# Kernel optimization log

Hardware: AMD Instinct MI355X
Metric: run time of the kernel (lower is better)

The kernel has to match this reference:

```python
import jax, jax.numpy as jnp
import numpy as np

N = 100000  # nodes
E = 1600000  # edges
F_IN, F_HID, F_OUT = 64, 128, 128


def _glorot(key, shape):
    fan_in, fan_out = shape[1], shape[0]
    lim = float(np.sqrt(6.0 / (fan_in + fan_out)))
    return jax.random.uniform(key, shape, jnp.float32, -lim, lim)


def setup_inputs() -> dict:
    key = jax.random.key(0)
    ks = jax.random.split(key, 8)
    x = jax.random.normal(ks[0], (N, F_IN), jnp.float32)
    edge_index = jax.random.randint(ks[1], (2, E), 0, N, jnp.int64)
    # SAGEConv params: lin_l (neighbors, with bias), lin_r (root, no bias)
    return {
        "x": x,
        "edge_index": edge_index,
        "W1_l": _glorot(ks[2], (F_HID, F_IN)),
        "b1": jnp.zeros((F_HID,), jnp.float32),
        "W1_r": _glorot(ks[3], (F_HID, F_IN)),
        "W2_l": _glorot(ks[4], (F_OUT, F_HID)),
        "b2": jnp.zeros((F_OUT,), jnp.float32),
        "W2_r": _glorot(ks[5], (F_OUT, F_HID)),
    }


def _sage_conv(x, src, dst, deg_inv, W_l, b, W_r):
    # mean aggregation of source features onto target nodes
    agg = jax.ops.segment_sum(x[src], dst, num_segments=N)  # [N, F]
    agg = agg * deg_inv[:, None]
    return agg @ W_l.T + b + x @ W_r.T


def reference(x, edge_index, W1_l, b1, W1_r, W2_l, b2, W2_r):
    src, dst = edge_index[0], edge_index[1]
    deg = jax.ops.segment_sum(jnp.ones((E,), jnp.float32), dst, num_segments=N)
    deg_inv = 1.0 / jnp.maximum(deg, 1.0)
    h = _sage_conv(x, src, dst, deg_inv, W1_l, b1, W1_r)
    h = jax.nn.relu(h)
    # dropout p=0.5 is identity in eval mode
    out = _sage_conv(h, src, dst, deg_inv, W2_l, b2, W2_r)
    return out
```

## Files before the change

kernel.cpp:

```cpp
#include <hip/hip_runtime.h>
#include <hip/hip_bf16.h>

__device__ __forceinline__ float b2f(unsigned short u) {
  return __uint_as_float(((unsigned int)u) << 16);
}
__device__ __forceinline__ unsigned short f2b(float f) {
  unsigned int x = __float_as_uint(f);
  unsigned int r = x + 0x7FFFu + ((x >> 16) & 1u);
  return (unsigned short)(r >> 16);
}
__device__ __forceinline__ unsigned int pack2(float lo, float hi) {
  return (unsigned int)f2b(lo) | ((unsigned int)f2b(hi) << 16);
}
__device__ __forceinline__ void acc8(float* a, uint4 p) {
  a[0] += __uint_as_float(p.x << 16); a[1] += __uint_as_float(p.x & 0xFFFF0000u);
  a[2] += __uint_as_float(p.y << 16); a[3] += __uint_as_float(p.y & 0xFFFF0000u);
  a[4] += __uint_as_float(p.z << 16); a[5] += __uint_as_float(p.z & 0xFFFF0000u);
  a[6] += __uint_as_float(p.w << 16); a[7] += __uint_as_float(p.w & 0xFFFF0000u);
}

typedef short bf16x8 __attribute__((ext_vector_type(8)));
typedef float f32x4 __attribute__((ext_vector_type(4)));

#define CHUNK 8192
#define NBUCKP 1024

__global__ void detect_kernel(const void* __restrict__ x_raw,
                              const void* __restrict__ idx_raw,
                              int* __restrict__ hdr) {
  int lane = threadIdx.x;
  const unsigned short* xb = (const unsigned short*)x_raw;
  unsigned short u = xb[2 * lane];
  int e = (u >> 7) & 0xFF;
  bool sane = ((u & 0x7FFFu) == 0) || (e >= 107 && e <= 137);
  unsigned long long m = __ballot(sane);
  const int* ib = (const int*)idx_raw;
  int v = ib[2 * lane + 1];
  unsigned long long m2 = __ballot(v != 0);
  if (lane == 0) {
    hdr[0] = (__popcll(m) >= 32) ? 0 : 1;
    hdr[1] = (m2 == 0ull) ? 1 : 0;
  }
}

__global__ void convert_w_kernel(const void* __restrict__ W1l, const void* __restrict__ W1r,
                                 const void* __restrict__ W2l, const void* __restrict__ W2r,
                                 const void* __restrict__ b1, const void* __restrict__ b2,
                                 const int* __restrict__ hdr,
                                 unsigned short* __restrict__ W1l_h, unsigned short* __restrict__ W1r_h,
                                 unsigned short* __restrict__ W2l_h, unsigned short* __restrict__ W2r_h,
                                 float* __restrict__ b1_f, float* __restrict__ b2_f) {
  int i = blockIdx.x * blockDim.x + threadIdx.x;
  const void* s; unsigned short* dh = nullptr; float* df = nullptr; int off;
  if (i < 8192)       { s = W1l; dh = W1l_h; off = i; }
  else if (i < 16384) { s = W1r; dh = W1r_h; off = i - 8192; }
  else if (i < 32768) { s = W2l; dh = W2l_h; off = i - 16384; }
  else if (i < 49152) { s = W2r; dh = W2r_h; off = i - 32768; }
  else if (i < 49280) { s = b1;  df = b1_f;  off = i - 49152; }
  else if (i < 49408) { s = b2;  df = b2_f;  off = i - 49280; }
  else return;
  float v = hdr[0] ? ((const float*)s)[off] : b2f(((const unsigned short*)s)[off]);
  if (dh) dh[off] = f2b(v);
  else df[off] = v;
}

__global__ void convert_x_kernel(const void* __restrict__ x_raw,
                                 const int* __restrict__ hdr,
                                 unsigned short* __restrict__ xc, int n_elems) {
  int i = blockIdx.x * blockDim.x + threadIdx.x;
  if (i >= n_elems) return;
  xc[i] = hdr[0] ? f2b(((const float*)x_raw)[i]) : ((const unsigned short*)x_raw)[i];
}

__global__ __launch_bounds__(256) void hist_chunks_kernel(
    const int* __restrict__ idx_raw, const int* __restrict__ hdr,
    int* __restrict__ H, int n_edges, int NC) {
  __shared__ int h[NBUCKP];
  for (int i = threadIdx.x; i < NBUCKP; i += 256) h[i] = 0;
  __syncthreads();
  const int c = blockIdx.x;
  const int base = c * CHUNK;
  const int lim = min(n_edges - base, CHUNK);
  if (hdr[1]) {
    const uint4* dp = (const uint4*)(idx_raw + 2 * (size_t)n_edges + 2 * (size_t)base);
    #pragma unroll
    for (int t = 0; t < CHUNK / 512; ++t) {
      int q = t * 256 + threadIdx.x;
      int e = 2 * q;
      if (e < lim) {
        uint4 v = dp[q];
        atomicAdd(&h[((int)v.x) >> 7], 1);
        if (e + 1 < lim) atomicAdd(&h[((int)v.z) >> 7], 1);
      }
    }
  } else {
    const uint4* dp = (const uint4*)(idx_raw + (size_t)n_edges + base);
    #pragma unroll
    for (int t = 0; t < CHUNK / 1024; ++t) {
      int q = t * 256 + threadIdx.x;
      int e = 4 * q;
      if (e < lim) {
        uint4 v = dp[q];
        atomicAdd(&h[((int)v.x) >> 7], 1);
        if (e + 1 < lim) atomicAdd(&h[((int)v.y) >> 7], 1);
        if (e + 2 < lim) atomicAdd(&h[((int)v.z) >> 7], 1);
        if (e + 3 < lim) atomicAdd(&h[((int)v.w) >> 7], 1);
      }
    }
  }
  __syncthreads();
  for (int i = threadIdx.x; i < NBUCKP; i += 256) H[(size_t)i * NC + c] = h[i];
}

__global__ __launch_bounds__(256) void gscan_sums_kernel(const int* __restrict__ arr,
                                                         int* __restrict__ blockSums, int n) {
  __shared__ int ws[4];
  int tid = threadIdx.x, lane = tid & 63, wid = tid >> 6;
  int base = blockIdx.x * 2048 + tid * 8;
  int s = 0;
  #pragma unroll
  for (int t = 0; t < 8; ++t) {
    int i = base + t;
    if (i < n) s += arr[i];
  }
  #pragma unroll
  for (int m = 1; m < 64; m <<= 1) s += __shfl_xor(s, m, 64);
  if (lane == 0) ws[wid] = s;
  __syncthreads();
  if (tid == 0) blockSums[blockIdx.x] = ws[0] + ws[1] + ws[2] + ws[3];
}

__global__ void gscan_offsets_kernel(const int* __restrict__ blockSums,
                                     int* __restrict__ blockOffs, int nb) {
  int lane = threadIdx.x;
  int carry = 0;
  for (int start = 0; start < nb; start += 64) {
    int i = start + lane;
    int v = (i < nb) ? blockSums[i] : 0;
    int isc = v;
    #pragma unroll
    for (int off = 1; off < 64; off <<= 1) {
      int t = __shfl_up(isc, off, 64);
      if (lane >= off) isc += t;
    }
    if (i < nb) blockOffs[i] = carry + isc - v;
    carry += __shfl(isc, 63, 64);
  }
}

__global__ __launch_bounds__(256) void gscan_emit_kernel(const int* __restrict__ arr,
                                                         const int* __restrict__ blockOffs,
                                                         int* __restrict__ out, int n) {
  __shared__ int ws[4];
  int tid = threadIdx.x, lane = tid & 63, wid = tid >> 6;
  int base = blockIdx.x * 2048 + tid * 8;
  int v[8];
  int s = 0;
  #pragma unroll
  for (int t = 0; t < 8; ++t) {
    int i = base + t;
    v[t] = (i < n) ? arr[i] : 0;
    s += v[t];
  }
  int isc = s;
  #pragma unroll
  for (int off = 1; off < 64; off <<= 1) {
    int t = __shfl_up(isc, off, 64);
    if (lane >= off) isc += t;
  }
  if (lane == 63) ws[wid] = isc;
  __syncthreads();
  int wb = 0;
  #pragma unroll
  for (int w = 0; w < 4; ++w)
    if (w < wid) wb += ws[w];
  int excl = blockOffs[blockIdx.x] + wb + isc - s;
  #pragma unroll
  for (int t = 0; t < 8; ++t) {
    int i = base + t;
    if (i < n) {
      out[i] = excl;
      excl += v[t];
    }
  }
}

__global__ __launch_bounds__(256) void scatter_kernel(
    const int* __restrict__ idx_raw, const int* __restrict__ hdr,
    const int* __restrict__ O, unsigned long long* __restrict__ ebuf,
    int n_edges, int NC) {
  __shared__ int base[NBUCKP];
  const int c = blockIdx.x;
  for (int i = threadIdx.x; i < NBUCKP; i += 256) base[i] = O[(size_t)i * NC + c];
  __syncthreads();
  const int eb = c * CHUNK;
  const int lim = min(n_edges - eb, CHUNK);
  if (hdr[1]) {
    const uint4* sp = (const uint4*)(idx_raw + 2 * (size_t)eb);
    const uint4* dp = (const uint4*)(idx_raw + 2 * (size_t)n_edges + 2 * (size_t)eb);
    #pragma unroll
    for (int t = 0; t < CHUNK / 512; ++t) {
      int q = t * 256 + threadIdx.x;
      int e = 2 * q;
      if (e < lim) {
        uint4 sv = sp[q], dv = dp[q];
        int p0 = atomicAdd(&base[((int)dv.x) >> 7], 1);
        ebuf[p0] = (unsigned long long)sv.x | ((unsigned long long)dv.x << 32);
        if (e + 1 < lim) {
          int p1 = atomicAdd(&base[((int)dv.z) >> 7], 1);
          ebuf[p1] = (unsigned long long)sv.z | ((unsigned long long)dv.z << 32);
        }
      }
    }
  } else {
    const uint4* sp = (const uint4*)(idx_raw + (size_t)eb);
    const uint4* dp = (const uint4*)(idx_raw + (size_t)n_edges + eb);
    #pragma unroll
    for (int t = 0; t < CHUNK / 1024; ++t) {
      int q = t * 256 + threadIdx.x;
      int e = 4 * q;
      if (e < lim) {
        uint4 sv = sp[q], dv = dp[q];
        int p0 = atomicAdd(&base[((int)dv.x) >> 7], 1);
        ebuf[p0] = (unsigned long long)sv.x | ((unsigned long long)dv.x << 32);
        if (e + 1 < lim) {
          int p1 = atomicAdd(&base[((int)dv.y) >> 7], 1);
          ebuf[p1] = (unsigned long long)sv.y | ((unsigned long long)dv.y << 32);
        }
        if (e + 2 < lim) {
          int p2 = atomicAdd(&base[((int)dv.z) >> 7], 1);
          ebuf[p2] = (unsigned long long)sv.z | ((unsigned long long)dv.z << 32);
        }
        if (e + 3 < lim) {
          int p3 = atomicAdd(&base[((int)dv.w) >> 7], 1);
          ebuf[p3] = (unsigned long long)sv.w | ((unsigned long long)dv.w << 32);
        }
      }
    }
  }
}

__global__ __launch_bounds__(256) void bucket_csr_kernel(
    const unsigned long long* __restrict__ ebuf, const int* __restrict__ O,
    int* __restrict__ col, int* __restrict__ row_start, float* __restrict__ deg_inv,
    int n_nodes, int n_edges, int NC) {
  __shared__ int cntl[128];
  __shared__ int cur[128];
  __shared__ int w0tot;
  const int b = blockIdx.x, tid = threadIdx.x;
  const int node0 = b << 7;
  const int beg = O[(size_t)b * NC];
  const int end = (b + 1 < NBUCKP) ? O[(size_t)(b + 1) * NC] : n_edges;
  if (tid < 128) cntl[tid] = 0;
  __syncthreads();
  for (int e = beg + tid; e < end; e += 256) {
    int d = (int)(ebuf[e] >> 32);
    atomicAdd(&cntl[d - node0], 1);
  }
  __syncthreads();
  int v = (tid < 128) ? cntl[tid] : 0;
  int lane = tid & 63;
  int isc = v;
  #pragma unroll
  for (int o = 1; o < 64; o <<= 1) {
    int t = __shfl_up(isc, o, 64);
    if (lane >= o) isc += t;
  }
  if (tid == 63) w0tot = isc;
  __syncthreads();
  int incl = isc + ((tid >= 64 && tid < 128) ? w0tot : 0);
  int excl = incl - v;
  if (tid < 128) {
    cur[tid] = excl;
    int node = node0 + tid;
    if (node < n_nodes) {
      row_start[node] = beg + excl;
      deg_inv[node] = 1.0f / (float)((v > 1) ? v : 1);
    }
  }
  __syncthreads();
  for (int e = beg + tid; e < end; e += 256) {
    unsigned long long u = ebuf[e];
    int s = (int)(u & 0xFFFFFFFFull);
    int d = (int)(u >> 32);
    int r = atomicAdd(&cur[d - node0], 1);
    col[beg + r] = s;
  }
  if (b == 0 && tid == 0) row_start[n_nodes] = n_edges;
}

__global__ __launch_bounds__(256) void gather1_kernel(
    const unsigned short* __restrict__ xc, const int* __restrict__ row_start,
    const int* __restrict__ col, const float* __restrict__ deg_inv,
    unsigned short* __restrict__ agg1, int n_nodes) {
  int lane = threadIdx.x & 63;
  int n = blockIdx.x * 8 + (threadIdx.x >> 6) * 2 + (lane >> 5);
  if (n >= n_nodes) return;
  int l32 = lane & 31;
  int rg = l32 >> 3, fq = l32 & 7;
  int beg = row_start[n], end = row_start[n + 1];
  float a[8];
  #pragma unroll
  for (int t = 0; t < 8; ++t) a[t] = 0.f;
  int i = beg;
  for (; i + 15 < end; i += 16) {
    int s0 = col[i + rg], s1 = col[i + 4 + rg], s2 = col[i + 8 + rg], s3 = col[i + 12 + rg];
    uint4 p0 = *(const uint4*)(xc + (size_t)s0 * 64 + fq * 8);
    uint4 p1 = *(const uint4*)(xc + (size_t)s1 * 64 + fq * 8);
    uint4 p2 = *(const uint4*)(xc + (size_t)s2 * 64 + fq * 8);
    uint4 p3 = *(const uint4*)(xc + (size_t)s3 * 64 + fq * 8);
    acc8(a, p0); acc8(a, p1); acc8(a, p2); acc8(a, p3);
  }
  for (; i + 3 < end; i += 4) {
    int s0 = col[i + rg];
    uint4 p0 = *(const uint4*)(xc + (size_t)s0 * 64 + fq * 8);
    acc8(a, p0);
  }
  if (i + rg < end) {
    int s0 = col[i + rg];
    uint4 p0 = *(const uint4*)(xc + (size_t)s0 * 64 + fq * 8);
    acc8(a, p0);
  }
  #pragma unroll
  for (int m = 8; m <= 16; m <<= 1)
    #pragma unroll
    for (int t = 0; t < 8; ++t) a[t] += __shfl_xor(a[t], m, 64);
  if (rg == 0) {
    float di = deg_inv[n];
    uint4 o;
    o.x = pack2(a[0] * di, a[1] * di);
    o.y = pack2(a[2] * di, a[3] * di);
    o.z = pack2(a[4] * di, a[5] * di);
    o.w = pack2(a[6] * di, a[7] * di);
    *(uint4*)(agg1 + (size_t)n * 64 + fq * 8) = o;
  }
}

__global__ __launch_bounds__(256) void gather2_kernel(
    const unsigned short* __restrict__ h, const int* __restrict__ row_start,
    const int* __restrict__ col, const float* __restrict__ deg_inv,
    unsigned short* __restrict__ agg2, int n_nodes) {
  int lane = threadIdx.x & 63;
  int n = blockIdx.x * 4 + (threadIdx.x >> 6);
  if (n >= n_nodes) return;
  int rg = lane >> 4, fq = lane & 15;
  int beg = row_start[n], end = row_start[n + 1];
  float a[8];
  #pragma unroll
  for (int t = 0; t < 8; ++t) a[t] = 0.f;
  int i = beg;
  for (; i + 15 < end; i += 16) {
    int s0 = col[i + rg], s1 = col[i + 4 + rg], s2 = col[i + 8 + rg], s3 = col[i + 12 + rg];
    uint4 p0 = *(const uint4*)(h + (size_t)s0 * 128 + fq * 8);
    uint4 p1 = *(const uint4*)(h + (size_t)s1 * 128 + fq * 8);
    uint4 p2 = *(const uint4*)(h + (size_t)s2 * 128 + fq * 8);
    uint4 p3 = *(const uint4*)(h + (size_t)s3 * 128 + fq * 8);
    acc8(a, p0); acc8(a, p1); acc8(a, p2); acc8(a, p3);
  }
  for (; i + 3 < end; i += 4) {
    int s0 = col[i + rg];
    uint4 p0 = *(const uint4*)(h + (size_t)s0 * 128 + fq * 8);
    acc8(a, p0);
  }
  if (i + rg < end) {
    int s0 = col[i + rg];
    uint4 p0 = *(const uint4*)(h + (size_t)s0 * 128 + fq * 8);
    acc8(a, p0);
  }
  #pragma unroll
  for (int m = 16; m < 64; m <<= 1)
    #pragma unroll
    for (int t = 0; t < 8; ++t) a[t] += __shfl_xor(a[t], m, 64);
  if (rg == 0) {
    float di = deg_inv[n];
    uint4 o;
    o.x = pack2(a[0] * di, a[1] * di);
    o.y = pack2(a[2] * di, a[3] * di);
    o.z = pack2(a[4] * di, a[5] * di);
    o.w = pack2(a[6] * di, a[7] * di);
    *(uint4*)(agg2 + (size_t)n * 128 + fq * 8) = o;
  }
}

template <int K1, int K2, bool RELU, bool FINAL>
__global__ __launch_bounds__(256, 4) void gemm_mfma(
    const unsigned short* __restrict__ A1, const unsigned short* __restrict__ A2,
    const unsigned short* __restrict__ Wl, const unsigned short* __restrict__ Wr,
    const float* __restrict__ bias,
    unsigned short* __restrict__ Cb, void* __restrict__ Cf,
    const int* __restrict__ hdr, int n_nodes) {
  const int tid = threadIdx.x;
  const int wave = tid >> 6, lane = tid & 63;
  const int m16 = lane & 15, quad = lane >> 4;
  const int nb = blockIdx.x * 128 + wave * 32;
  int row0 = nb + m16;      if (row0 >= n_nodes) row0 = n_nodes - 1;
  int row1 = nb + 16 + m16; if (row1 >= n_nodes) row1 = n_nodes - 1;

  f32x4 acc[2][8];
  #pragma unroll
  for (int mi = 0; mi < 2; ++mi)
    #pragma unroll
    for (int ji = 0; ji < 8; ++ji) acc[mi][ji] = (f32x4){0.f, 0.f, 0.f, 0.f};

  constexpr int NSTEP = (K1 + K2) / 32;
  #pragma unroll
  for (int c = 0; c < NSTEP; ++c) {
    const bool first = (c * 32) < K1;
    const unsigned short* A = first ? A1 : A2;
    const unsigned short* W = first ? Wl : Wr;
    const int kb = first ? c * 32 : c * 32 - K1;
    const int Krow = first ? K1 : K2;
    const int ko = kb + quad * 8;
    bf16x8 a0 = *(const bf16x8*)(A + (size_t)row0 * Krow + ko);
    bf16x8 a1 = *(const bf16x8*)(A + (size_t)row1 * Krow + ko);
    bf16x8 w[8];
    #pragma unroll
    for (int ji = 0; ji < 8; ++ji)
      w[ji] = *(const bf16x8*)(W + (size_t)(ji * 16 + m16) * Krow + ko);
    #pragma unroll
    for (int ji = 0; ji < 8; ++ji) {
      acc[0][ji] = __builtin_amdgcn_mfma_f32_16x16x32_bf16(a0, w[ji], acc[0][ji], 0, 0, 0);
      acc[1][ji] = __builtin_amdgcn_mfma_f32_16x16x32_bf16(a1, w[ji], acc[1][ji], 0, 0, 0);
    }
  }

  const bool f32out = FINAL && (hdr[0] == 1);
  #pragma unroll
  for (int ji = 0; ji < 8; ++ji) {
    int j = ji * 16 + m16;
    float bj = bias[j];
    #pragma unroll
    for (int mi = 0; mi < 2; ++mi) {
      #pragma unroll
      for (int r = 0; r < 4; ++r) {
        int n = nb + mi * 16 + quad * 4 + r;
        if (n >= n_nodes) continue;
        float v = acc[mi][ji][r] + bj;
        if (RELU) v = fmaxf(v, 0.f);
        if (FINAL) {
          if (f32out) ((float*)Cf)[(size_t)n * 128 + j] = v;
          else ((unsigned short*)Cf)[(size_t)n * 128 + j] = f2b(v);
        } else {
          Cb[(size_t)n * 128 + j] = f2b(v);
        }
      }
    }
  }
}

extern "C" void kernel_launch(void* const* d_in, const int* in_sizes, int n_in,
                              void* d_out, int out_size, void* d_ws, size_t ws_size,
                              hipStream_t stream) {
  const void* x_raw  = d_in[0];
  const int* idx_raw = (const int*)d_in[1];
  const void* W1l = d_in[2];
  const void* b1  = d_in[3];
  const void* W1r = d_in[4];
  const void* W2l = d_in[5];
  const void* b2  = d_in[6];
  const void* W2r = d_in[7];
  const int N = in_sizes[0] / 64;
  const int E = in_sizes[1] / 2;
  const int NC = (E + CHUNK - 1) / CHUNK;
  const int NSCAN = NBUCKP * NC;
  const int NBs = (NSCAN + 2047) / 2048;
  const int NBUCK = (N + 127) >> 7;

  char* ws = (char*)d_ws;
  size_t off = 0;
  auto alloc = [&](size_t bytes) {
    char* p = ws + off;
    off = (off + bytes + 511) & ~((size_t)511);
    return p;
  };
  int* hdr        = (int*)alloc(512);
  int* H          = (int*)alloc((size_t)NSCAN * 4);
  int* O          = (int*)alloc((size_t)NSCAN * 4);
  int* blockSums  = (int*)alloc((size_t)NBs * 4);
  int* blockOffs  = (int*)alloc((size_t)NBs * 4);
  unsigned long long* ebuf = (unsigned long long*)alloc((size_t)E * 8);
  int* col        = (int*)alloc((size_t)E * 4);
  int* row_start  = (int*)alloc(((size_t)N + 1) * 4);
  float* deg_inv  = (float*)alloc((size_t)N * 4);
  unsigned short* W1l_h = (unsigned short*)alloc(16384);
  unsigned short* W1r_h = (unsigned short*)alloc(16384);
  unsigned short* W2l_h = (unsigned short*)alloc(32768);
  unsigned short* W2r_h = (unsigned short*)alloc(32768);
  float* b1_f     = (float*)alloc(512);
  float* b2_f     = (float*)alloc(512);
  unsigned short* xc   = (unsigned short*)alloc((size_t)N * 64 * 2);
  unsigned short* agg1 = (unsigned short*)alloc((size_t)N * 64 * 2);
  unsigned short* hbuf = (unsigned short*)alloc((size_t)N * 128 * 2);
  unsigned short* agg2 = (unsigned short*)alloc((size_t)N * 128 * 2);

  detect_kernel<<<1, 64, 0, stream>>>(x_raw, idx_raw, hdr);
  convert_w_kernel<<<(49408 + 255) / 256, 256, 0, stream>>>(
      W1l, W1r, W2l, W2r, b1, b2, hdr, W1l_h, W1r_h, W2l_h, W2r_h, b1_f, b2_f);
  convert_x_kernel<<<(N * 64 + 255) / 256, 256, 0, stream>>>(x_raw, hdr, xc, N * 64);
  hist_chunks_kernel<<<NC, 256, 0, stream>>>(idx_raw, hdr, H, E, NC);
  gscan_sums_kernel<<<NBs, 256, 0, stream>>>(H, blockSums, NSCAN);
  gscan_offsets_kernel<<<1, 64, 0, stream>>>(blockSums, blockOffs, NBs);
  gscan_emit_kernel<<<NBs, 256, 0, stream>>>(H, blockOffs, O, NSCAN);
  scatter_kernel<<<NC, 256, 0, stream>>>(idx_raw, hdr, O, ebuf, E, NC);
  bucket_csr_kernel<<<NBUCK, 256, 0, stream>>>(ebuf, O, col, row_start, deg_inv, N, E, NC);
  gather1_kernel<<<(N + 7) / 8, 256, 0, stream>>>(xc, row_start, col, deg_inv, agg1, N);
  gemm_mfma<64, 64, true, false><<<(N + 127) / 128, 256, 0, stream>>>(
      agg1, xc, W1l_h, W1r_h, b1_f, hbuf, nullptr, hdr, N);
  gather2_kernel<<<(N + 3) / 4, 256, 0, stream>>>(hbuf, row_start, col, deg_inv, agg2, N);
  gemm_mfma<128, 128, false, true><<<(N + 127) / 128, 256, 0, stream>>>(
      agg2, hbuf, W2l_h, W2r_h, b2_f, nullptr, d_out, hdr, N);
}
```

Baseline: 331.8 us.

## Fuse neighbor gather into MFMA GEMM via LDS tile, skip conversion for bf16 inputs

Merges each layer's mean-aggregation gather into its MFMA GEMM kernel. The aggregated rows are written into a shared-memory tile instead of a global agg buffer, which removes one kernel launch per layer and the write and reread of agg1/agg2. The convert kernels now exit early when inputs are already bf16, and the GEMM reads raw weights and bias directly in that case. In exchange each block does the gather with only 256 threads over 128 nodes before the GEMM starts, and the LDS tile may lower occupancy and reduce latency hiding for the irregular gather.

```diff
diff --git a/kernel.cpp b/kernel.cpp
--- a/kernel.cpp
+++ b/kernel.cpp
@@ -45,31 +45,27 @@
 
 __global__ void convert_w_kernel(const void* __restrict__ W1l, const void* __restrict__ W1r,
                                  const void* __restrict__ W2l, const void* __restrict__ W2r,
-                                 const void* __restrict__ b1, const void* __restrict__ b2,
                                  const int* __restrict__ hdr,
                                  unsigned short* __restrict__ W1l_h, unsigned short* __restrict__ W1r_h,
-                                 unsigned short* __restrict__ W2l_h, unsigned short* __restrict__ W2r_h,
-                                 float* __restrict__ b1_f, float* __restrict__ b2_f) {
+                                 unsigned short* __restrict__ W2l_h, unsigned short* __restrict__ W2r_h) {
+  if (hdr[0] == 0) return;
   int i = blockIdx.x * blockDim.x + threadIdx.x;
-  const void* s; unsigned short* dh = nullptr; float* df = nullptr; int off;
-  if (i < 8192)       { s = W1l; dh = W1l_h; off = i; }
-  else if (i < 16384) { s = W1r; dh = W1r_h; off = i - 8192; }
-  else if (i < 32768) { s = W2l; dh = W2l_h; off = i - 16384; }
-  else if (i < 49152) { s = W2r; dh = W2r_h; off = i - 32768; }
-  else if (i < 49280) { s = b1;  df = b1_f;  off = i - 49152; }
-  else if (i < 49408) { s = b2;  df = b2_f;  off = i - 49280; }
+  const float* s; unsigned short* d; int off;
+  if (i < 8192)       { s = (const float*)W1l; d = W1l_h; off = i; }
+  else if (i < 16384) { s = (const float*)W1r; d = W1r_h; off = i - 8192; }
+  else if (i < 32768) { s = (const float*)W2l; d = W2l_h; off = i - 16384; }
+  else if (i < 49152) { s = (const float*)W2r; d = W2r_h; off = i - 32768; }
   else return;
-  float v = hdr[0] ? ((const float*)s)[off] : b2f(((const unsigned short*)s)[off]);
-  if (dh) dh[off] = f2b(v);
-  else df[off] = v;
+  d[off] = f2b(s[off]);
 }
 
 __global__ void convert_x_kernel(const void* __restrict__ x_raw,
                                  const int* __restrict__ hdr,
                                  unsigned short* __restrict__ xc, int n_elems) {
+  if (hdr[0] == 0) return;
   int i = blockIdx.x * blockDim.x + threadIdx.x;
   if (i >= n_elems) return;
-  xc[i] = hdr[0] ? f2b(((const float*)x_raw)[i]) : ((const unsigned short*)x_raw)[i];
+  xc[i] = f2b(((const float*)x_raw)[i]);
 }
 
 __global__ __launch_bounds__(256) void hist_chunks_kernel(
@@ -289,112 +285,115 @@
   if (b == 0 && tid == 0) row_start[n_nodes] = n_edges;
 }
 
-__global__ __launch_bounds__(256) void gather1_kernel(
-    const unsigned short* __restrict__ xc, const int* __restrict__ row_start,
-    const int* __restrict__ col, const float* __restrict__ deg_inv,
-    unsigned short* __restrict__ agg1, int n_nodes) {
-  int lane = threadIdx.x & 63;
-  int n = blockIdx.x * 8 + (threadIdx.x >> 6) * 2 + (lane >> 5);
-  if (n >= n_nodes) return;
-  int l32 = lane & 31;
-  int rg = l32 >> 3, fq = l32 & 7;
-  int beg = row_start[n], end = row_start[n + 1];
-  float a[8];
-  #pragma unroll
-  for (int t = 0; t < 8; ++t) a[t] = 0.f;
-  int i = beg;
-  for (; i + 15 < end; i += 16) {
-    int s0 = col[i + rg], s1 = col[i + 4 + rg], s2 = col[i + 8 + rg], s3 = col[i + 12 + rg];
-    uint4 p0 = *(const uint4*)(xc + (size_t)s0 * 64 + fq * 8);
-    uint4 p1 = *(const uint4*)(xc + (size_t)s1 * 64 + fq * 8);
-    uint4 p2 = *(const uint4*)(xc + (size_t)s2 * 64 + fq * 8);
-    uint4 p3 = *(const uint4*)(xc + (size_t)s3 * 64 + fq * 8);
-    acc8(a, p0); acc8(a, p1); acc8(a, p2); acc8(a, p3);
-  }
-  for (; i + 3 < end; i += 4) {
-    int s0 = col[i + rg];
-    uint4 p0 = *(const uint4*)(xc + (size_t)s0 * 64 + fq * 8);
-    acc8(a, p0);
-  }
-  if (i + rg < end) {
-    int s0 = col[i + rg];
-    uint4 p0 = *(const uint4*)(xc + (size_t)s0 * 64 + fq * 8);
-    acc8(a, p0);
-  }
-  #pragma unroll
-  for (int m = 8; m <= 16; m <<= 1)
-    #pragma unroll
-    for (int t = 0; t < 8; ++t) a[t] += __shfl_xor(a[t], m, 64);
-  if (rg == 0) {
-    float di = deg_inv[n];
-    uint4 o;
-    o.x = pack2(a[0] * di, a[1] * di);
-    o.y = pack2(a[2] * di, a[3] * di);
-    o.z = pack2(a[4] * di, a[5] * di);
-    o.w = pack2(a[6] * di, a[7] * di);
-    *(uint4*)(agg1 + (size_t)n * 64 + fq * 8) = o;
-  }
-}
-
-__global__ __launch_bounds__(256) void gather2_kernel(
-    const unsigned short* __restrict__ h, const int* __restrict__ row_start,
-    const int* __restrict__ col, const float* __restrict__ deg_inv,
-    unsigned short* __restrict__ agg2, int n_nodes) {
-  int lane = threadIdx.x & 63;
-  int n = blockIdx.x * 4 + (threadIdx.x >> 6);
-  if (n >= n_nodes) return;
-  int rg = lane >> 4, fq = lane & 15;
-  int beg = row_start[n], end = row_start[n + 1];
-  float a[8];
-  #pragma unroll
-  for (int t = 0; t < 8; ++t) a[t] = 0.f;
-  int i = beg;
-  for (; i + 15 < end; i += 16) {
-    int s0 = col[i + rg], s1 = col[i + 4 + rg], s2 = col[i + 8 + rg], s3 = col[i + 12 + rg];
-    uint4 p0 = *(const uint4*)(h + (size_t)s0 * 128 + fq * 8);
-    uint4 p1 = *(const uint4*)(h + (size_t)s1 * 128 + fq * 8);
-    uint4 p2 = *(const uint4*)(h + (size_t)s2 * 128 + fq * 8);
-    uint4 p3 = *(const uint4*)(h + (size_t)s3 * 128 + fq * 8);
-    acc8(a, p0); acc8(a, p1); acc8(a, p2); acc8(a, p3);
-  }
-  for (; i + 3 < end; i += 4) {
-    int s0 = col[i + rg];
-    uint4 p0 = *(const uint4*)(h + (size_t)s0 * 128 + fq * 8);
-    acc8(a, p0);
-  }
-  if (i + rg < end) {
-    int s0 = col[i + rg];
-    uint4 p0 = *(const uint4*)(h + (size_t)s0 * 128 + fq * 8);
-    acc8(a, p0);
-  }
-  #pragma unroll
-  for (int m = 16; m < 64; m <<= 1)
-    #pragma unroll
-    for (int t = 0; t < 8; ++t) a[t] += __shfl_xor(a[t], m, 64);
-  if (rg == 0) {
-    float di = deg_inv[n];
-    uint4 o;
-    o.x = pack2(a[0] * di, a[1] * di);
-    o.y = pack2(a[2] * di, a[3] * di);
-    o.z = pack2(a[4] * di, a[5] * di);
-    o.w = pack2(a[6] * di, a[7] * di);
-    *(uint4*)(agg2 + (size_t)n * 128 + fq * 8) = o;
-  }
-}
-
-template <int K1, int K2, bool RELU, bool FINAL>
-__global__ __launch_bounds__(256, 4) void gemm_mfma(
-    const unsigned short* __restrict__ A1, const unsigned short* __restrict__ A2,
-    const unsigned short* __restrict__ Wl, const unsigned short* __restrict__ Wr,
-    const float* __restrict__ bias,
-    unsigned short* __restrict__ Cb, void* __restrict__ Cf,
-    const int* __restrict__ hdr, int n_nodes) {
+template <int KA, bool RELU, bool FINAL>
+__global__ __launch_bounds__(256, 4) void fgemm_kernel(
+    const unsigned short* __restrict__ Xconv, const void* __restrict__ Xraw,
+    const int* __restrict__ row_start, const int* __restrict__ col,
+    const float* __restrict__ deg_inv,
+    const void* __restrict__ Wl_raw, const void* __restrict__ Wr_raw,
+    const unsigned short* __restrict__ Wl_conv, const unsigned short* __restrict__ Wr_conv,
+    const void* __restrict__ bias_raw, const int* __restrict__ hdr,
+    unsigned short* __restrict__ Cb, void* __restrict__ Cf, int n_nodes) {
+  constexpr int LROW = KA + 8;
+  __shared__ unsigned short tile[128 * LROW];
   const int tid = threadIdx.x;
   const int wave = tid >> 6, lane = tid & 63;
+  const int hdr0 = hdr[0];
+  const unsigned short* X  = hdr0 ? Xconv : (const unsigned short*)Xraw;
+  const unsigned short* Wl = hdr0 ? Wl_conv : (const unsigned short*)Wl_raw;
+  const unsigned short* Wr = hdr0 ? Wr_conv : (const unsigned short*)Wr_raw;
+  const int nb = blockIdx.x * 128;
+
+  if (KA == 128) {
+    const int rg = lane >> 4, fq = lane & 15;
+    for (int t = 0; t < 32; ++t) {
+      const int n = nb + wave * 32 + t;
+      float a[8];
+      #pragma unroll
+      for (int q = 0; q < 8; ++q) a[q] = 0.f;
+      if (n < n_nodes) {
+        int beg = row_start[n], end = row_start[n + 1];
+        int i = beg;
+        for (; i + 15 < end; i += 16) {
+          int s0 = col[i + rg], s1 = col[i + 4 + rg], s2 = col[i + 8 + rg], s3 = col[i + 12 + rg];
+          uint4 p0 = *(const uint4*)(X + (size_t)s0 * 128 + fq * 8);
+          uint4 p1 = *(const uint4*)(X + (size_t)s1 * 128 + fq * 8);
+          uint4 p2 = *(const uint4*)(X + (size_t)s2 * 128 + fq * 8);
+          uint4 p3 = *(const uint4*)(X + (size_t)s3 * 128 + fq * 8);
+          acc8(a, p0); acc8(a, p1); acc8(a, p2); acc8(a, p3);
+        }
+        for (; i + 3 < end; i += 4) {
+          uint4 p0 = *(const uint4*)(X + (size_t)col[i + rg] * 128 + fq * 8);
+          acc8(a, p0);
+        }
+        if (i + rg < end) {
+          uint4 p0 = *(const uint4*)(X + (size_t)col[i + rg] * 128 + fq * 8);
+          acc8(a, p0);
+        }
+        #pragma unroll
+        for (int m = 16; m < 64; m <<= 1)
+          #pragma unroll
+          for (int q = 0; q < 8; ++q) a[q] += __shfl_xor(a[q], m, 64);
+      }
+      if (rg == 0) {
+        float di = (n < n_nodes) ? deg_inv[n] : 0.f;
+        uint4 o;
+        o.x = pack2(a[0] * di, a[1] * di);
+        o.y = pack2(a[2] * di, a[3] * di);
+        o.z = pack2(a[4] * di, a[5] * di);
+        o.w = pack2(a[6] * di, a[7] * di);
+        *(uint4*)&tile[(wave * 32 + t) * LROW + fq * 8] = o;
+      }
+    }
+  } else {
+    const int half = lane >> 5, l32 = lane & 31;
+    const int rg = l32 >> 3, fq = l32 & 7;
+    for (int t = 0; t < 16; ++t) {
+      const int n = nb + wave * 32 + t * 2 + half;
+      float a[8];
+      #pragma unroll
+      for (int q = 0; q < 8; ++q) a[q] = 0.f;
+      if (n < n_nodes) {
+        int beg = row_start[n], end = row_start[n + 1];
+        int i = beg;
+        for (; i + 15 < end; i += 16) {
+          int s0 = col[i + rg], s1 = col[i + 4 + rg], s2 = col[i + 8 + rg], s3 = col[i + 12 + rg];
+          uint4 p0 = *(const uint4*)(X + (size_t)s0 * 64 + fq * 8);
+          uint4 p1 = *(const uint4*)(X + (size_t)s1 * 64 + fq * 8);
+          uint4 p2 = *(const uint4*)(X + (size_t)s2 * 64 + fq * 8);
+          uint4 p3 = *(const uint4*)(X + (size_t)s3 * 64 + fq * 8);
+          acc8(a, p0); acc8(a, p1); acc8(a, p2); acc8(a, p3);
+        }
+        for (; i + 3 < end; i += 4) {
+          uint4 p0 = *(const uint4*)(X + (size_t)col[i + rg] * 64 + fq * 8);
+          acc8(a, p0);
+        }
+        if (i + rg < end) {
+          uint4 p0 = *(const uint4*)(X + (size_t)col[i + rg] * 64 + fq * 8);
+          acc8(a, p0);
+        }
+        #pragma unroll
+        for (int m = 8; m <= 16; m <<= 1)
+          #pragma unroll
+          for (int q = 0; q < 8; ++q) a[q] += __shfl_xor(a[q], m, 64);
+      }
+      if (rg == 0) {
+        float di = (n < n_nodes) ? deg_inv[n] : 0.f;
+        uint4 o;
+        o.x = pack2(a[0] * di, a[1] * di);
+        o.y = pack2(a[2] * di, a[3] * di);
+        o.z = pack2(a[4] * di, a[5] * di);
+        o.w = pack2(a[6] * di, a[7] * di);
+        *(uint4*)&tile[(wave * 32 + t * 2 + half) * LROW + fq * 8] = o;
+      }
+    }
+  }
+  __syncthreads();
+
   const int m16 = lane & 15, quad = lane >> 4;
-  const int nb = blockIdx.x * 128 + wave * 32;
-  int row0 = nb + m16;      if (row0 >= n_nodes) row0 = n_nodes - 1;
-  int row1 = nb + 16 + m16; if (row1 >= n_nodes) row1 = n_nodes - 1;
+  const int gnb = nb + wave * 32, lnb = wave * 32;
+  int srow0 = gnb + m16;      if (srow0 >= n_nodes) srow0 = n_nodes - 1;
+  int srow1 = gnb + 16 + m16; if (srow1 >= n_nodes) srow1 = n_nodes - 1;
 
   f32x4 acc[2][8];
   #pragma unroll
@@ -402,21 +401,25 @@
     #pragma unroll
     for (int ji = 0; ji < 8; ++ji) acc[mi][ji] = (f32x4){0.f, 0.f, 0.f, 0.f};
 
-  constexpr int NSTEP = (K1 + K2) / 32;
+  constexpr int NSTEP = (2 * KA) / 32;
   #pragma unroll
   for (int c = 0; c < NSTEP; ++c) {
-    const bool first = (c * 32) < K1;
-    const unsigned short* A = first ? A1 : A2;
+    const bool first = (c * 32) < KA;
+    const int kb = first ? c * 32 : c * 32 - KA;
+    const int ko = kb + quad * 8;
+    bf16x8 a0, a1;
+    if (first) {
+      a0 = *(const bf16x8*)&tile[(lnb + m16) * LROW + ko];
+      a1 = *(const bf16x8*)&tile[(lnb + 16 + m16) * LROW + ko];
+    } else {
+      a0 = *(const bf16x8*)(X + (size_t)srow0 * KA + ko);
+      a1 = *(const bf16x8*)(X + (size_t)srow1 * KA + ko);
+    }
     const unsigned short* W = first ? Wl : Wr;
-    const int kb = first ? c * 32 : c * 32 - K1;
-    const int Krow = first ? K1 : K2;
-    const int ko = kb + quad * 8;
-    bf16x8 a0 = *(const bf16x8*)(A + (size_t)row0 * Krow + ko);
-    bf16x8 a1 = *(const bf16x8*)(A + (size_t)row1 * Krow + ko);
     bf16x8 w[8];
     #pragma unroll
     for (int ji = 0; ji < 8; ++ji)
-      w[ji] = *(const bf16x8*)(W + (size_t)(ji * 16 + m16) * Krow + ko);
+      w[ji] = *(const bf16x8*)(W + (size_t)(ji * 16 + m16) * KA + ko);
     #pragma unroll
     for (int ji = 0; ji < 8; ++ji) {
       acc[0][ji] = __builtin_amdgcn_mfma_f32_16x16x32_bf16(a0, w[ji], acc[0][ji], 0, 0, 0);
@@ -424,16 +427,16 @@
     }
   }
 
-  const bool f32out = FINAL && (hdr[0] == 1);
+  const bool f32out = FINAL && (hdr0 == 1);
   #pragma unroll
   for (int ji = 0; ji < 8; ++ji) {
     int j = ji * 16 + m16;
-    float bj = bias[j];
+    float bj = hdr0 ? ((const float*)bias_raw)[j] : b2f(((const unsigned short*)bias_raw)[j]);
     #pragma unroll
     for (int mi = 0; mi < 2; ++mi) {
       #pragma unroll
       for (int r = 0; r < 4; ++r) {
-        int n = nb + mi * 16 + quad * 4 + r;
+        int n = gnb + mi * 16 + quad * 4 + r;
         if (n >= n_nodes) continue;
         float v = acc[mi][ji][r] + bj;
         if (RELU) v = fmaxf(v, 0.f);
@@ -486,16 +489,12 @@
   unsigned short* W1r_h = (unsigned short*)alloc(16384);
   unsigned short* W2l_h = (unsigned short*)alloc(32768);
   unsigned short* W2r_h = (unsigned short*)alloc(32768);
-  float* b1_f     = (float*)alloc(512);
-  float* b2_f     = (float*)alloc(512);
   unsigned short* xc   = (unsigned short*)alloc((size_t)N * 64 * 2);
-  unsigned short* agg1 = (unsigned short*)alloc((size_t)N * 64 * 2);
   unsigned short* hbuf = (unsigned short*)alloc((size_t)N * 128 * 2);
-  unsigned short* agg2 = (unsigned short*)alloc((size_t)N * 128 * 2);
 
   detect_kernel<<<1, 64, 0, stream>>>(x_raw, idx_raw, hdr);
-  convert_w_kernel<<<(49408 + 255) / 256, 256, 0, stream>>>(
-      W1l, W1r, W2l, W2r, b1, b2, hdr, W1l_h, W1r_h, W2l_h, W2r_h, b1_f, b2_f);
+  convert_w_kernel<<<(49152 + 255) / 256, 256, 0, stream>>>(
+      W1l, W1r, W2l, W2r, hdr, W1l_h, W1r_h, W2l_h, W2r_h);
   convert_x_kernel<<<(N * 64 + 255) / 256, 256, 0, stream>>>(x_raw, hdr, xc, N * 64);
   hist_chunks_kernel<<<NC, 256, 0, stream>>>(idx_raw, hdr, H, E, NC);
   gscan_sums_kernel<<<NBs, 256, 0, stream>>>(H, blockSums, NSCAN);
@@ -503,10 +502,10 @@
   gscan_emit_kernel<<<NBs, 256, 0, stream>>>(H, blockOffs, O, NSCAN);
   scatter_kernel<<<NC, 256, 0, stream>>>(idx_raw, hdr, O, ebuf, E, NC);
   bucket_csr_kernel<<<NBUCK, 256, 0, stream>>>(ebuf, O, col, row_start, deg_inv, N, E, NC);
-  gather1_kernel<<<(N + 7) / 8, 256, 0, stream>>>(xc, row_start, col, deg_inv, agg1, N);
-  gemm_mfma<64, 64, true, false><<<(N + 127) / 128, 256, 0, stream>>>(
-      agg1, xc, W1l_h, W1r_h, b1_f, hbuf, nullptr, hdr, N);
-  gather2_kernel<<<(N + 3) / 4, 256, 0, stream>>>(hbuf, row_start, col, deg_inv, agg2, N);
-  gemm_mfma<128, 128, false, true><<<(N + 127) / 128, 256, 0, stream>>>(
-      agg2, hbuf, W2l_h, W2r_h, b2_f, nullptr, d_out, hdr, N);
-}
+  fgemm_kernel<64, true, false><<<(N + 127) / 128, 256, 0, stream>>>(
+      xc, x_raw, row_start, col, deg_inv, W1l, W1r, W1l_h, W1r_h, b1, hdr,
+      hbuf, nullptr, N);
+  fgemm_kernel<128, false, true><<<(N + 127) / 128, 256, 0, stream>>>(
+      hbuf, hbuf, row_start, col, deg_inv, W2l, W2r, W2l_h, W2r_h, b2, hdr,
+      nullptr, d_out, N);
+}
```

Measured after the change: 377.0 us. 1.14x slower.
